# Kernel optimization log

Measured on AMD Instinct MI355X. Metric: run time of the kernel, lower is better.

## Reference

```python
import jax, jax.numpy as jnp
import numpy as np
from functools import partial

RES = 512          # image resolution (source uses 1024; scaled for CPU baseline)
BLOB_COUNT = 2048  # number of Gaussian blobs (source uses 4096)
CHUNK = 64         # blobs processed per scan step to bound intermediates


def setup_inputs() -> dict:
    key = jax.random.key(0)
    k_pos, k_scale, k_rot, k_col = jax.random.split(key, 4)
    pos = jax.random.uniform(k_pos, (BLOB_COUNT, 2))                      # blob centers in [0,1]^2
    scale = 0.005 + 0.05 * jax.random.uniform(k_scale, (BLOB_COUNT, 2))   # per-axis std dev
    rot = 2.0 * jnp.pi * jax.random.uniform(k_rot, (BLOB_COUNT, 1))       # rotation angle
    color = jax.random.uniform(k_col, (BLOB_COUNT, 3))                    # rgb intensity
    blobs = jnp.concatenate([pos, scale, rot, color], axis=-1).astype(jnp.float32)  # [N, 8]
    return {"blobs": blobs}


def _splat(blobs):
    H = W = RES
    # pixel centers in normalized [0,1] coords
    ys = (jnp.arange(H, dtype=jnp.float32) + 0.5) / H
    xs = (jnp.arange(W, dtype=jnp.float32) + 0.5) / W
    py, px = jnp.meshgrid(ys, xs, indexing="ij")  # [H, W]

    def body(img, chunk):  # chunk: [CHUNK, 8]
        pos = chunk[:, 0:2]
        sx = chunk[:, 2][:, None, None]
        sy = chunk[:, 3][:, None, None]
        rot = chunk[:, 4]
        color = chunk[:, 5:8]
        c = jnp.cos(rot)[:, None, None]
        s = jnp.sin(rot)[:, None, None]
        dx = px[None] - pos[:, 0][:, None, None]   # [C, H, W]
        dy = py[None] - pos[:, 1][:, None, None]
        xr = c * dx + s * dy                        # rotate into blob frame
        yr = -s * dx + c * dy
        g = jnp.exp(-0.5 * ((xr / sx) ** 2 + (yr / sy) ** 2))  # [C, H, W]
        img = img + jnp.einsum("chw,ck->hwk", g, color)
        return img, None

    img0 = jnp.zeros((H, W, 3), dtype=blobs.dtype)
    chunks = blobs.reshape(BLOB_COUNT // CHUNK, CHUNK, 8)
    img, _ = jax.lax.scan(jax.checkpoint(body), img0, chunks)
    return img


@jax.jit
def reference(blobs):
    return _splat(blobs)
```

## Files before the change

### kernel.cpp

```cpp
#include <hip/hip_runtime.h>
#include <math.h>

#define RES     512
#define NBLOB   2048
#define TILE_W  32
#define TILE_H  32
#define ROWS_T  8
#define TX_N    (RES / TILE_W)
#define TY_N    (RES / TILE_H)
#define CHUNK_B 256
#define NCHUNK  (NBLOB / CHUNK_B)
#define K_CONST   0.84932184f
#define SQRT_CULL 3.7416574f
#define HALFDIAG  0.0428132f

__device__ __forceinline__ float fast_exp2(float x) {
#if __has_builtin(__builtin_amdgcn_exp2f)
    return __builtin_amdgcn_exp2f(x);
#else
    return exp2f(x);
#endif
}

__global__ __launch_bounds__(256) void splat_kernel(const float* __restrict__ blobs,
                                                    float* __restrict__ out) {
    __shared__ int sh_cnt[NCHUNK];
    __shared__ float4 sh_p0[CHUNK_B];
    __shared__ float4 sh_p1[CHUNK_B];
    __shared__ float  sh_p2[CHUNK_B];

    const int tid = threadIdx.x;
    const int lane = tid & 63;
    const int tx = blockIdx.x;
    const int ty = blockIdx.y;

    if (tid < NCHUNK) sh_cnt[tid] = 0;

    const int x  = tx * TILE_W + (tid & 31);
    const int y0 = ty * TILE_H + (tid >> 5);
    const float fx  = (x + 0.5f) * (1.0f / RES);
    const float fy0 = (y0 + 0.5f) * (1.0f / RES);
    const float DY  = (float)ROWS_T * (1.0f / RES);

    const float cxT = (tx * TILE_W + 16.0f) * (1.0f / RES);
    const float cyT = (ty * TILE_H + 16.0f) * (1.0f / RES);

    float ar0 = 0.f, ag0 = 0.f, ab0 = 0.f;
    float ar1 = 0.f, ag1 = 0.f, ab1 = 0.f;
    float ar2 = 0.f, ag2 = 0.f, ab2 = 0.f;
    float ar3 = 0.f, ag3 = 0.f, ab3 = 0.f;

    __syncthreads();

    for (int c = 0; c < NCHUNK; ++c) {
        const int j = c * CHUNK_B + tid;
        const float4 b0 = *(const float4*)(blobs + j * 8);
        const float4 b1 = *(const float4*)(blobs + j * 8 + 4);
        const float sx = b0.z, sy = b0.w;
        float sn, cn;
        __sincosf(b1.x, &sn, &cn);
        const float isx = K_CONST / sx;
        const float isy = K_CONST / sy;
        const float ma =  cn * isx;
        const float mb =  sn * isx;
        const float md = -sn * isy;
        const float me =  cn * isy;
        const float opn = K_CONST / fminf(sx, sy);
        const float rt  = SQRT_CULL + opn * HALFDIAG;
        const float dxc = cxT - b0.x;
        const float dyc = cyT - b0.y;
        const float uc = ma * dxc + mb * dyc;
        const float vc = md * dxc + me * dyc;
        const bool hit = fmaf(uc, uc, vc * vc) <= rt * rt;

        const unsigned long long mask = __ballot(hit);
        const int total = __popcll(mask);
        int base = 0;
        if (lane == 0 && total > 0) base = atomicAdd(&sh_cnt[c], total);
        base = __builtin_amdgcn_readfirstlane(base);
        if (hit) {
            const int pos = base + __popcll(mask & ((1ull << lane) - 1ull));
            sh_p0[pos] = make_float4(b0.x, b0.y, ma, mb);
            sh_p1[pos] = make_float4(md, me, b1.y, b1.z);
            sh_p2[pos] = b1.w;
        }
        __syncthreads();

        const int n = sh_cnt[c];
        #pragma unroll 4
        for (int k = 0; k < n; ++k) {
            const float4 p0 = sh_p0[k];
            const float4 p1 = sh_p1[k];
            const float  cb = sh_p2[k];
            const float dx = fx - p0.x;
            const float dy = fy0 - p0.y;
            const float bD = p0.w * DY;
            const float eD = p1.y * DY;
            float u = p0.z * dx + p0.w * dy;
            float v = p1.x * dx + p1.y * dy;

            const float g0 = fast_exp2(-fmaf(u, u, v * v));
            u += bD; v += eD;
            const float g1 = fast_exp2(-fmaf(u, u, v * v));
            u += bD; v += eD;
            const float g2 = fast_exp2(-fmaf(u, u, v * v));
            u += bD; v += eD;
            const float g3 = fast_exp2(-fmaf(u, u, v * v));

            ar0 += g0 * p1.z;  ag0 += g0 * p1.w;  ab0 += g0 * cb;
            ar1 += g1 * p1.z;  ag1 += g1 * p1.w;  ab1 += g1 * cb;
            ar2 += g2 * p1.z;  ag2 += g2 * p1.w;  ab2 += g2 * cb;
            ar3 += g3 * p1.z;  ag3 += g3 * p1.w;  ab3 += g3 * cb;
        }
        __syncthreads();
    }

    const int b0i = (y0 * RES + x) * 3;
    out[b0i + 0] = ar0;  out[b0i + 1] = ag0;  out[b0i + 2] = ab0;
    const int b1i = ((y0 + ROWS_T) * RES + x) * 3;
    out[b1i + 0] = ar1;  out[b1i + 1] = ag1;  out[b1i + 2] = ab1;
    const int b2i = ((y0 + 2 * ROWS_T) * RES + x) * 3;
    out[b2i + 0] = ar2;  out[b2i + 1] = ag2;  out[b2i + 2] = ab2;
    const int b3i = ((y0 + 3 * ROWS_T) * RES + x) * 3;
    out[b3i + 0] = ar3;  out[b3i + 1] = ag3;  out[b3i + 2] = ab3;
}

extern "C" void kernel_launch(void* const* d_in, const int* in_sizes, int n_in,
                              void* d_out, int out_size, void* d_ws, size_t ws_size,
                              hipStream_t stream) {
    const float* blobs = (const float*)d_in[0];
    float* out = (float*)d_out;
    (void)d_ws; (void)ws_size;

    hipLaunchKernelGGL(splat_kernel, dim3(TX_N, TY_N), dim3(256), 0, stream,
                       blobs, out);
}
```

Measured before the change: 78.63 us.

## Halve tile height, double-buffer blob lists and prefetch next chunk

Tile height drops from 32 to 16, so each thread accumulates two rows instead of four and the grid doubles to 512 blocks. The culling radius is retightened to match the smaller tile half-diagonal. Shared compacted blob lists are double-buffered, which removes the trailing barrier of each chunk, and the next chunk's blob data is loaded from global memory into registers before the compute loop. In exchange, blobs that overlap several tiles are evaluated more times across blocks, and LDS use doubles.

```diff
diff --git a/kernel.cpp b/kernel.cpp
--- a/kernel.cpp
+++ b/kernel.cpp
@@ -4,15 +4,15 @@
 #define RES     512
 #define NBLOB   2048
 #define TILE_W  32
-#define TILE_H  32
+#define TILE_H  16
 #define ROWS_T  8
 #define TX_N    (RES / TILE_W)
 #define TY_N    (RES / TILE_H)
 #define CHUNK_B 256
 #define NCHUNK  (NBLOB / CHUNK_B)
 #define K_CONST   0.84932184f
-#define SQRT_CULL 3.7416574f
-#define HALFDIAG  0.0428132f
+#define SQRT_CULL 3.4641016f
+#define HALFDIAG  0.0336327f
 
 __device__ __forceinline__ float fast_exp2(float x) {
 #if __has_builtin(__builtin_amdgcn_exp2f)
@@ -25,9 +25,9 @@
 __global__ __launch_bounds__(256) void splat_kernel(const float* __restrict__ blobs,
                                                     float* __restrict__ out) {
     __shared__ int sh_cnt[NCHUNK];
-    __shared__ float4 sh_p0[CHUNK_B];
-    __shared__ float4 sh_p1[CHUNK_B];
-    __shared__ float  sh_p2[CHUNK_B];
+    __shared__ float4 sh_p0[2][CHUNK_B];
+    __shared__ float4 sh_p1[2][CHUNK_B];
+    __shared__ float  sh_p2[2][CHUNK_B];
 
     const int tid = threadIdx.x;
     const int lane = tid & 63;
@@ -43,22 +43,20 @@
     const float DY  = (float)ROWS_T * (1.0f / RES);
 
     const float cxT = (tx * TILE_W + 16.0f) * (1.0f / RES);
-    const float cyT = (ty * TILE_H + 16.0f) * (1.0f / RES);
+    const float cyT = (ty * TILE_H + 8.0f) * (1.0f / RES);
 
     float ar0 = 0.f, ag0 = 0.f, ab0 = 0.f;
     float ar1 = 0.f, ag1 = 0.f, ab1 = 0.f;
-    float ar2 = 0.f, ag2 = 0.f, ab2 = 0.f;
-    float ar3 = 0.f, ag3 = 0.f, ab3 = 0.f;
+
+    float4 rb0 = *(const float4*)(blobs + (size_t)tid * 8);
+    float4 rb1 = *(const float4*)(blobs + (size_t)tid * 8 + 4);
 
     __syncthreads();
 
     for (int c = 0; c < NCHUNK; ++c) {
-        const int j = c * CHUNK_B + tid;
-        const float4 b0 = *(const float4*)(blobs + j * 8);
-        const float4 b1 = *(const float4*)(blobs + j * 8 + 4);
-        const float sx = b0.z, sy = b0.w;
+        const float sx = rb0.z, sy = rb0.w;
         float sn, cn;
-        __sincosf(b1.x, &sn, &cn);
+        __sincosf(rb1.x, &sn, &cn);
         const float isx = K_CONST / sx;
         const float isy = K_CONST / sy;
         const float ma =  cn * isx;
@@ -67,8 +65,8 @@
         const float me =  cn * isy;
         const float opn = K_CONST / fminf(sx, sy);
         const float rt  = SQRT_CULL + opn * HALFDIAG;
-        const float dxc = cxT - b0.x;
-        const float dyc = cyT - b0.y;
+        const float dxc = cxT - rb0.x;
+        const float dyc = cyT - rb0.y;
         const float uc = ma * dxc + mb * dyc;
         const float vc = md * dxc + me * dyc;
         const bool hit = fmaf(uc, uc, vc * vc) <= rt * rt;
@@ -78,51 +76,47 @@
         int base = 0;
         if (lane == 0 && total > 0) base = atomicAdd(&sh_cnt[c], total);
         base = __builtin_amdgcn_readfirstlane(base);
+        const int buf = c & 1;
         if (hit) {
             const int pos = base + __popcll(mask & ((1ull << lane) - 1ull));
-            sh_p0[pos] = make_float4(b0.x, b0.y, ma, mb);
-            sh_p1[pos] = make_float4(md, me, b1.y, b1.z);
-            sh_p2[pos] = b1.w;
+            sh_p0[buf][pos] = make_float4(rb0.x, rb0.y, ma, mb);
+            sh_p1[buf][pos] = make_float4(md, me, rb1.y, rb1.z);
+            sh_p2[buf][pos] = rb1.w;
         }
+
+        const int jn = (c + 1 < NCHUNK ? c + 1 : c) * CHUNK_B + tid;
+        const float4 nb0 = *(const float4*)(blobs + (size_t)jn * 8);
+        const float4 nb1 = *(const float4*)(blobs + (size_t)jn * 8 + 4);
+
         __syncthreads();
 
         const int n = sh_cnt[c];
         #pragma unroll 4
         for (int k = 0; k < n; ++k) {
-            const float4 p0 = sh_p0[k];
-            const float4 p1 = sh_p1[k];
-            const float  cb = sh_p2[k];
+            const float4 p0 = sh_p0[buf][k];
+            const float4 p1 = sh_p1[buf][k];
+            const float  cb = sh_p2[buf][k];
             const float dx = fx - p0.x;
             const float dy = fy0 - p0.y;
-            const float bD = p0.w * DY;
-            const float eD = p1.y * DY;
             float u = p0.z * dx + p0.w * dy;
             float v = p1.x * dx + p1.y * dy;
 
             const float g0 = fast_exp2(-fmaf(u, u, v * v));
-            u += bD; v += eD;
+            u += p0.w * DY; v += p1.y * DY;
             const float g1 = fast_exp2(-fmaf(u, u, v * v));
-            u += bD; v += eD;
-            const float g2 = fast_exp2(-fmaf(u, u, v * v));
-            u += bD; v += eD;
-            const float g3 = fast_exp2(-fmaf(u, u, v * v));
 
             ar0 += g0 * p1.z;  ag0 += g0 * p1.w;  ab0 += g0 * cb;
             ar1 += g1 * p1.z;  ag1 += g1 * p1.w;  ab1 += g1 * cb;
-            ar2 += g2 * p1.z;  ag2 += g2 * p1.w;  ab2 += g2 * cb;
-            ar3 += g3 * p1.z;  ag3 += g3 * p1.w;  ab3 += g3 * cb;
         }
-        __syncthreads();
+
+        rb0 = nb0;
+        rb1 = nb1;
     }
 
     const int b0i = (y0 * RES + x) * 3;
     out[b0i + 0] = ar0;  out[b0i + 1] = ag0;  out[b0i + 2] = ab0;
     const int b1i = ((y0 + ROWS_T) * RES + x) * 3;
     out[b1i + 0] = ar1;  out[b1i + 1] = ag1;  out[b1i + 2] = ab1;
-    const int b2i = ((y0 + 2 * ROWS_T) * RES + x) * 3;
-    out[b2i + 0] = ar2;  out[b2i + 1] = ag2;  out[b2i + 2] = ab2;
-    const int b3i = ((y0 + 3 * ROWS_T) * RES + x) * 3;
-    out[b3i + 0] = ar3;  out[b3i + 1] = ag3;  out[b3i + 2] = ab3;
 }
 
 extern "C" void kernel_launch(void* const* d_in, const int* in_sizes, int n_in,
```

Result: faster. 73.52 us (-6.5%).
